# Kernel optimization log

Measured on AMD Instinct MI355X. Metric: run time of the kernel, lower is better.

Reference implementation:

```python
import jax, jax.numpy as jnp
import numpy as np

WS = 8
NH = 8
EPS = 1e-5

def layer_norm(x, g, b):
    m = jnp.mean(x, axis=-1, keepdims=True)
    v = jnp.mean(jnp.square(x - m), axis=-1, keepdims=True)
    return (x - m) * jax.lax.rsqrt(v + EPS) * g + b

def setup_inputs() -> dict:
    key = jax.random.key(0)
    ks = jax.random.split(key, 12)
    C = 512
    s = 1.0 / np.sqrt(C)
    return {
        "x": jax.random.normal(ks[0], (16, C, 96, 96), dtype=jnp.float32),
        "Wqkv": jax.random.normal(ks[1], (C, 3 * C), dtype=jnp.float32) * s,
        "bqkv": jnp.zeros((3 * C,), dtype=jnp.float32),
        "Wo": jax.random.normal(ks[2], (C, C), dtype=jnp.float32) * s,
        "bo": jnp.zeros((C,), dtype=jnp.float32),
        "g1": jnp.ones((C,), dtype=jnp.float32),
        "beta1": jnp.zeros((C,), dtype=jnp.float32),
        "W1": jax.random.normal(ks[3], (C, C), dtype=jnp.float32) * s,
        "bf1": jnp.zeros((C,), dtype=jnp.float32),
        "W2": jax.random.normal(ks[4], (C, C), dtype=jnp.float32) * s,
        "bf2": jnp.zeros((C,), dtype=jnp.float32),
        "g2": jnp.ones((C,), dtype=jnp.float32),
        "beta2": jnp.zeros((C,), dtype=jnp.float32),
    }

def _block(t, Wqkv, bqkv, Wo, bo, g1, beta1, W1, bf1, W2, bf2, g2, beta2):
    # t: [N, L, C]  (windows of L = ws*ws tokens)
    N, L, C = t.shape
    dh = C // NH
    qkv = t @ Wqkv + bqkv                       # [N, L, 3C]
    q, k, v = jnp.split(qkv, 3, axis=-1)
    q = q.reshape(N, L, NH, dh).transpose(0, 2, 1, 3)  # [N,H,L,dh]
    k = k.reshape(N, L, NH, dh).transpose(0, 2, 1, 3)
    v = v.reshape(N, L, NH, dh).transpose(0, 2, 1, 3)
    scores = jnp.einsum('nhqd,nhkd->nhqk', q, k) / jnp.sqrt(jnp.float32(dh))
    attn = jax.nn.softmax(scores, axis=-1)
    o = jnp.einsum('nhqk,nhkd->nhqd', attn, v)  # [N,H,L,dh]
    o = o.transpose(0, 2, 1, 3).reshape(N, L, C) @ Wo + bo
    x1 = layer_norm(t + o, g1, beta1)
    f = jax.nn.relu(x1 @ W1 + bf1) @ W2 + bf2
    return layer_norm(x1 + f, g2, beta2)

def reference(x, Wqkv, bqkv, Wo, bo, g1, beta1, W1, bf1, W2, bf2, g2, beta2):
    B, C, H, W = x.shape
    ws = WS
    # H, W divisible by ws (pad amounts are 0 for chosen shapes)
    nh, nw = H // ws, W // ws
    xw = x.reshape(B, C, nh, ws, nw, ws)
    xw = xw.transpose(0, 2, 4, 3, 5, 1).reshape(B * nh * nw, ws * ws, C)
    y = _block(xw, Wqkv, bqkv, Wo, bo, g1, beta1, W1, bf1, W2, bf2, g2, beta2)
    y = y.reshape(B, nh, nw, ws, ws, C)
    y = y.transpose(0, 5, 1, 3, 2, 4).reshape(B, C, H, W)
    return y
```

## Files before the change

### kernel.cpp

```cpp
#include <hip/hip_runtime.h>

typedef short short8 __attribute__((ext_vector_type(8)));
typedef float f32x4 __attribute__((ext_vector_type(4)));

#define NWIN 2304
#define CP 520
#define LP2 136
#define VTP 72
#define SMEM_BYTES 124416

static __device__ __forceinline__ unsigned short f2bf(float f) {
  unsigned int u = __float_as_uint(f);
  u += 0x7FFFu + ((u >> 16) & 1u);
  return (unsigned short)(u >> 16);
}
static __device__ __forceinline__ float bf2f(unsigned short s) {
  return __uint_as_float(((unsigned int)s) << 16);
}
static __device__ __forceinline__ f32x4 mfma16(short8 a, short8 b, f32x4 c) {
  return __builtin_amdgcn_mfma_f32_16x16x32_bf16(a, b, c, 0, 0, 0);
}
static __device__ __forceinline__ short8 lds8(const unsigned short* p) {
  return *reinterpret_cast<const short8*>(p);
}

__global__ void transpose_cvt_kernel(const float* __restrict__ in,
                                     unsigned short* __restrict__ out,
                                     int K, int N) {
  __shared__ float tile[32][33];
  int bn = blockIdx.x * 32, bk = blockIdx.y * 32;
  int tx = threadIdx.x & 31, ty = threadIdx.x >> 5;
#pragma unroll
  for (int r = 0; r < 32; r += 8)
    tile[ty + r][tx] = in[(size_t)(bk + ty + r) * N + bn + tx];
  __syncthreads();
#pragma unroll
  for (int r = 0; r < 32; r += 8)
    out[(size_t)(bn + ty + r) * K + bk + tx] = f2bf(tile[tx][ty + r]);
}

__global__ __launch_bounds__(512, 2)
void swin_fused(const float* __restrict__ x,
                const unsigned short* __restrict__ WqkvT,
                const float* __restrict__ bqkv,
                const unsigned short* __restrict__ WoT,
                const float* __restrict__ bo,
                const float* __restrict__ g1, const float* __restrict__ beta1,
                const unsigned short* __restrict__ W1T,
                const float* __restrict__ bf1,
                const unsigned short* __restrict__ W2T,
                const float* __restrict__ bf2,
                const float* __restrict__ g2, const float* __restrict__ beta2,
                float* __restrict__ out) {
  extern __shared__ unsigned char smem[];
  unsigned short* sT  = (unsigned short*)smem;
  unsigned short* sQ  = (unsigned short*)(smem + 66560);
  unsigned short* sK  = (unsigned short*)(smem + 83968);
  unsigned short* sVt = (unsigned short*)(smem + 101376);
  unsigned short* sH  = sK;
  float* sSum  = (float*)(smem + 119808);
  float* sSq   = (float*)(smem + 121856);
  float* sMean = (float*)(smem + 123904);
  float* sRstd = (float*)(smem + 124160);

  const int tid = threadIdx.x;
  const int wvid = tid >> 6, lane = tid & 63;
  const int l16 = lane & 15, lg = lane >> 4;

  const int wid = (blockIdx.x & 7) * 288 + (blockIdx.x >> 3);
  const int b = wid / 144, rem = wid % 144;
  const int h0 = (rem / 12) * 8, w0 = (rem % 12) * 8;
  const float* xb = x + (size_t)b * 512 * 9216 + (size_t)h0 * 96 + w0;
  float* ob = out + (size_t)b * 512 * 9216 + (size_t)h0 * 96 + w0;

  const int c2 = wvid * 16 + l16;
  const int hh = wvid >> 2;
  const int mt4 = wvid & 3;
  const int ycol0 = wvid * 64;

#pragma unroll
  for (int it = 0; it < 16; ++it) {
    int gid = it * 512 + tid;
    int c = gid >> 4, hr = (gid >> 1) & 7, wq = gid & 1;
    float4 v = *reinterpret_cast<const float4*>(xb + (size_t)c * 9216 + hr * 96 + wq * 4);
    int tok = hr * 8 + wq * 4;
    sT[(tok + 0) * CP + c] = f2bf(v.x);
    sT[(tok + 1) * CP + c] = f2bf(v.y);
    sT[(tok + 2) * CP + c] = f2bf(v.z);
    sT[(tok + 3) * CP + c] = f2bf(v.w);
  }
  __syncthreads();

  f32x4 Yacc[4][4] = {};

  for (int hp = 0; hp < 4; ++hp) {
    {
      const unsigned short* bq = WqkvT + (size_t)(hp * 128 + c2) * 512;
      const unsigned short* bk = bq + (size_t)512 * 512;
      const unsigned short* bv = bq + (size_t)1024 * 512;
      f32x4 acc[3][4] = {};
      short8 qw[4], kw[4], vw[4];
#pragma unroll
      for (int p = 0; p < 4; ++p) {
        int ko = p * 32 + lg * 8;
        qw[p] = *(const short8*)(bq + ko);
        kw[p] = *(const short8*)(bk + ko);
        vw[p] = *(const short8*)(bv + ko);
      }
#pragma unroll
      for (int ks = 0; ks < 16; ++ks) {
        const int ko = ks * 32 + lg * 8;
        short8 cq = qw[ks & 3], ck = kw[ks & 3], cv = vw[ks & 3];
        if (ks < 12) {
          int ko2 = (ks + 4) * 32 + lg * 8;
          qw[ks & 3] = *(const short8*)(bq + ko2);
          kw[ks & 3] = *(const short8*)(bk + ko2);
          vw[ks & 3] = *(const short8*)(bv + ko2);
        }
        short8 a0 = lds8(&sT[(l16) * CP + ko]);
        short8 a1 = lds8(&sT[(16 + l16) * CP + ko]);
        short8 a2 = lds8(&sT[(32 + l16) * CP + ko]);
        short8 a3 = lds8(&sT[(48 + l16) * CP + ko]);
        acc[0][0] = mfma16(a0, cq, acc[0][0]);
        acc[0][1] = mfma16(a1, cq, acc[0][1]);
        acc[0][2] = mfma16(a2, cq, acc[0][2]);
        acc[0][3] = mfma16(a3, cq, acc[0][3]);
        acc[1][0] = mfma16(a0, ck, acc[1][0]);
        acc[1][1] = mfma16(a1, ck, acc[1][1]);
        acc[1][2] = mfma16(a2, ck, acc[1][2]);
        acc[1][3] = mfma16(a3, ck, acc[1][3]);
        acc[2][0] = mfma16(a0, cv, acc[2][0]);
        acc[2][1] = mfma16(a1, cv, acc[2][1]);
        acc[2][2] = mfma16(a2, cv, acc[2][2]);
        acc[2][3] = mfma16(a3, cv, acc[2][3]);
      }
      const float bqv = bqkv[hp * 128 + c2];
      const float bkv = bqkv[512 + hp * 128 + c2];
      const float bvv = bqkv[1024 + hp * 128 + c2];
#pragma unroll
      for (int mt = 0; mt < 4; ++mt) {
        int tok0 = mt * 16 + lg * 4;
#pragma unroll
        for (int r = 0; r < 4; ++r) {
          sQ[(tok0 + r) * LP2 + c2] = f2bf((acc[0][mt][r] + bqv) * 0.125f);
          sK[(tok0 + r) * LP2 + c2] = f2bf(acc[1][mt][r] + bkv);
        }
        ushort4 pk;
        pk.x = f2bf(acc[2][mt][0] + bvv);
        pk.y = f2bf(acc[2][mt][1] + bvv);
        pk.z = f2bf(acc[2][mt][2] + bvv);
        pk.w = f2bf(acc[2][mt][3] + bvv);
        *reinterpret_cast<ushort4*>(&sVt[c2 * VTP + tok0]) = pk;
      }
    }
    __syncthreads();

    {
      f32x4 sc[4] = {};
#pragma unroll
      for (int ks = 0; ks < 2; ++ks) {
        int ko = hh * 64 + ks * 32 + lg * 8;
        short8 a  = lds8(&sQ[(mt4 * 16 + l16) * LP2 + ko]);
        short8 b0 = lds8(&sK[(l16) * LP2 + ko]);
        short8 b1 = lds8(&sK[(16 + l16) * LP2 + ko]);
        short8 b2 = lds8(&sK[(32 + l16) * LP2 + ko]);
        short8 b3 = lds8(&sK[(48 + l16) * LP2 + ko]);
        sc[0] = mfma16(a, b0, sc[0]);
        sc[1] = mfma16(a, b1, sc[1]);
        sc[2] = mfma16(a, b2, sc[2]);
        sc[3] = mfma16(a, b3, sc[3]);
      }
#pragma unroll
      for (int r = 0; r < 4; ++r) {
        float m = fmaxf(fmaxf(sc[0][r], sc[1][r]), fmaxf(sc[2][r], sc[3][r]));
        m = fmaxf(m, __shfl_xor(m, 1));
        m = fmaxf(m, __shfl_xor(m, 2));
        m = fmaxf(m, __shfl_xor(m, 4));
        m = fmaxf(m, __shfl_xor(m, 8));
        float e0 = __expf(sc[0][r] - m), e1 = __expf(sc[1][r] - m);
        float e2 = __expf(sc[2][r] - m), e3 = __expf(sc[3][r] - m);
        float s = e0 + e1 + e2 + e3;
        s += __shfl_xor(s, 1);
        s += __shfl_xor(s, 2);
        s += __shfl_xor(s, 4);
        s += __shfl_xor(s, 8);
        float inv = 1.0f / s;
        int row = mt4 * 16 + lg * 4 + r;
        sQ[row * LP2 + hh * 64 + l16]      = f2bf(e0 * inv);
        sQ[row * LP2 + hh * 64 + 16 + l16] = f2bf(e1 * inv);
        sQ[row * LP2 + hh * 64 + 32 + l16] = f2bf(e2 * inv);
        sQ[row * LP2 + hh * 64 + 48 + l16] = f2bf(e3 * inv);
      }
    }

    {
      f32x4 ov[4] = {};
#pragma unroll
      for (int ks = 0; ks < 2; ++ks) {
        int ko = ks * 32 + lg * 8;
        short8 a  = lds8(&sQ[(mt4 * 16 + l16) * LP2 + hh * 64 + ko]);
        short8 b0 = lds8(&sVt[(hh * 64 + l16) * VTP + ko]);
        short8 b1 = lds8(&sVt[(hh * 64 + 16 + l16) * VTP + ko]);
        short8 b2 = lds8(&sVt[(hh * 64 + 32 + l16) * VTP + ko]);
        short8 b3 = lds8(&sVt[(hh * 64 + 48 + l16) * VTP + ko]);
        ov[0] = mfma16(a, b0, ov[0]);
        ov[1] = mfma16(a, b1, ov[1]);
        ov[2] = mfma16(a, b2, ov[2]);
        ov[3] = mfma16(a, b3, ov[3]);
      }
#pragma unroll
      for (int r = 0; r < 4; ++r) {
        int row = mt4 * 16 + lg * 4 + r;
        sQ[row * LP2 + hh * 64 + l16]      = f2bf(ov[0][r]);
        sQ[row * LP2 + hh * 64 + 16 + l16] = f2bf(ov[1][r]);
        sQ[row * LP2 + hh * 64 + 32 + l16] = f2bf(ov[2][r]);
        sQ[row * LP2 + hh * 64 + 48 + l16] = f2bf(ov[3][r]);
      }
    }
    __syncthreads();

    {
      const unsigned short* wo0 = WoT + (size_t)(ycol0 + l16) * 512 + hp * 128;
      short8 wb[4][4];
#pragma unroll
      for (int ks = 0; ks < 4; ++ks)
#pragma unroll
        for (int nt = 0; nt < 4; ++nt)
          wb[ks][nt] = *(const short8*)(wo0 + (size_t)nt * 16 * 512 + ks * 32 + lg * 8);
#pragma unroll
      for (int ks = 0; ks < 4; ++ks) {
        int ko = ks * 32 + lg * 8;
        short8 a0 = lds8(&sQ[(l16) * LP2 + ko]);
        short8 a1 = lds8(&sQ[(16 + l16) * LP2 + ko]);
        short8 a2 = lds8(&sQ[(32 + l16) * LP2 + ko]);
        short8 a3 = lds8(&sQ[(48 + l16) * LP2 + ko]);
#pragma unroll
        for (int nt = 0; nt < 4; ++nt) {
          Yacc[0][nt] = mfma16(a0, wb[ks][nt], Yacc[0][nt]);
          Yacc[1][nt] = mfma16(a1, wb[ks][nt], Yacc[1][nt]);
          Yacc[2][nt] = mfma16(a2, wb[ks][nt], Yacc[2][nt]);
          Yacc[3][nt] = mfma16(a3, wb[ks][nt], Yacc[3][nt]);
        }
      }
    }
    __syncthreads();
  }

  {
#pragma unroll
    for (int nt = 0; nt < 4; ++nt) {
      int col = ycol0 + nt * 16 + l16;
      float bv = bo[col];
#pragma unroll
      for (int mt = 0; mt < 4; ++mt) {
        int row0 = mt * 16 + lg * 4;
#pragma unroll
        for (int r = 0; r < 4; ++r)
          Yacc[mt][nt][r] += bv + bf2f(sT[(row0 + r) * CP + col]);
      }
    }
#pragma unroll
    for (int mt = 0; mt < 4; ++mt) {
#pragma unroll
      for (int r = 0; r < 4; ++r) {
        float s = Yacc[mt][0][r] + Yacc[mt][1][r] + Yacc[mt][2][r] + Yacc[mt][3][r];
        float q = Yacc[mt][0][r] * Yacc[mt][0][r] + Yacc[mt][1][r] * Yacc[mt][1][r] +
                  Yacc[mt][2][r] * Yacc[mt][2][r] + Yacc[mt][3][r] * Yacc[mt][3][r];
        s += __shfl_xor(s, 1); s += __shfl_xor(s, 2);
        s += __shfl_xor(s, 4); s += __shfl_xor(s, 8);
        q += __shfl_xor(q, 1); q += __shfl_xor(q, 2);
        q += __shfl_xor(q, 4); q += __shfl_xor(q, 8);
        if (l16 == 0) {
          sSum[wvid * 64 + mt * 16 + lg * 4 + r] = s;
          sSq[wvid * 64 + mt * 16 + lg * 4 + r] = q;
        }
      }
    }
    __syncthreads();
    if (tid < 64) {
      float s = 0.f, q = 0.f;
#pragma unroll
      for (int w = 0; w < 8; ++w) { s += sSum[w * 64 + tid]; q += sSq[w * 64 + tid]; }
      float mean = s * (1.0f / 512.0f);
      float var = q * (1.0f / 512.0f) - mean * mean;
      sMean[tid] = mean;
      sRstd[tid] = rsqrtf(var + 1e-5f);
    }
    __syncthreads();
#pragma unroll
    for (int nt = 0; nt < 4; ++nt) {
      int col = ycol0 + nt * 16 + l16;
      float gv = g1[col], bv = beta1[col];
#pragma unroll
      for (int mt = 0; mt < 4; ++mt) {
        int row0 = mt * 16 + lg * 4;
#pragma unroll
        for (int r = 0; r < 4; ++r) {
          float xv = (Yacc[mt][nt][r] - sMean[row0 + r]) * sRstd[row0 + r] * gv + bv;
          sT[(row0 + r) * CP + col] = f2bf(xv);
        }
      }
    }
  }
  __syncthreads();

  f32x4 Facc[4][4] = {};
  for (int hc = 0; hc < 4; ++hc) {
    {
      const int hcol = hc * 128 + c2;
      const unsigned short* w1p = W1T + (size_t)hcol * 512;
      f32x4 u[4] = {};
      short8 wbuf[4];
#pragma unroll
      for (int p = 0; p < 4; ++p)
        wbuf[p] = *(const short8*)(w1p + p * 32 + lg * 8);
#pragma unroll
      for (int ks = 0; ks < 16; ++ks) {
        int ko = ks * 32 + lg * 8;
        short8 cw = wbuf[ks & 3];
        if (ks < 12)
          wbuf[ks & 3] = *(const short8*)(w1p + (ks + 4) * 32 + lg * 8);
        short8 a0 = lds8(&sT[(l16) * CP + ko]);
        short8 a1 = lds8(&sT[(16 + l16) * CP + ko]);
        short8 a2 = lds8(&sT[(32 + l16) * CP + ko]);
        short8 a3 = lds8(&sT[(48 + l16) * CP + ko]);
        u[0] = mfma16(a0, cw, u[0]);
        u[1] = mfma16(a1, cw, u[1]);
        u[2] = mfma16(a2, cw, u[2]);
        u[3] = mfma16(a3, cw, u[3]);
      }
      float bv = bf1[hcol];
#pragma unroll
      for (int mt = 0; mt < 4; ++mt) {
        int tok0 = mt * 16 + lg * 4;
#pragma unroll
        for (int r = 0; r < 4; ++r)
          sH[(tok0 + r) * LP2 + c2] = f2bf(fmaxf(u[mt][r] + bv, 0.0f));
      }
    }
    __syncthreads();
    {
      const unsigned short* w2p = W2T + (size_t)(ycol0 + l16) * 512 + hc * 128;
      short8 wb[4][4];
#pragma unroll
      for (int ks = 0; ks < 4; ++ks)
#pragma unroll
        for (int nt = 0; nt < 4; ++nt)
          wb[ks][nt] = *(const short8*)(w2p + (size_t)nt * 16 * 512 + ks * 32 + lg * 8);
#pragma unroll
      for (int ks = 0; ks < 4; ++ks) {
        int ko = ks * 32 + lg * 8;
        short8 a0 = lds8(&sH[(l16) * LP2 + ko]);
        short8 a1 = lds8(&sH[(16 + l16) * LP2 + ko]);
        short8 a2 = lds8(&sH[(32 + l16) * LP2 + ko]);
        short8 a3 = lds8(&sH[(48 + l16) * LP2 + ko]);
#pragma unroll
        for (int nt = 0; nt < 4; ++nt) {
          Facc[0][nt] = mfma16(a0, wb[ks][nt], Facc[0][nt]);
          Facc[1][nt] = mfma16(a1, wb[ks][nt], Facc[1][nt]);
          Facc[2][nt] = mfma16(a2, wb[ks][nt], Facc[2][nt]);
          Facc[3][nt] = mfma16(a3, wb[ks][nt], Facc[3][nt]);
        }
      }
    }
    __syncthreads();
  }

  {
#pragma unroll
    for (int nt = 0; nt < 4; ++nt) {
      int col = ycol0 + nt * 16 + l16;
      float bv = bf2[col];
#pragma unroll
      for (int mt = 0; mt < 4; ++mt) {
        int row0 = mt * 16 + lg * 4;
#pragma unroll
        for (int r = 0; r < 4; ++r)
          Facc[mt][nt][r] += bv + bf2f(sT[(row0 + r) * CP + col]);
      }
    }
#pragma unroll
    for (int mt = 0; mt < 4; ++mt) {
#pragma unroll
      for (int r = 0; r < 4; ++r) {
        float s = Facc[mt][0][r] + Facc[mt][1][r] + Facc[mt][2][r] + Facc[mt][3][r];
        float q = Facc[mt][0][r] * Facc[mt][0][r] + Facc[mt][1][r] * Facc[mt][1][r] +
                  Facc[mt][2][r] * Facc[mt][2][r] + Facc[mt][3][r] * Facc[mt][3][r];
        s += __shfl_xor(s, 1); s += __shfl_xor(s, 2);
        s += __shfl_xor(s, 4); s += __shfl_xor(s, 8);
        q += __shfl_xor(q, 1); q += __shfl_xor(q, 2);
        q += __shfl_xor(q, 4); q += __shfl_xor(q, 8);
        if (l16 == 0) {
          sSum[wvid * 64 + mt * 16 + lg * 4 + r] = s;
          sSq[wvid * 64 + mt * 16 + lg * 4 + r] = q;
        }
      }
    }
    __syncthreads();
    if (tid < 64) {
      float s = 0.f, q = 0.f;
#pragma unroll
      for (int w = 0; w < 8; ++w) { s += sSum[w * 64 + tid]; q += sSq[w * 64 + tid]; }
      float mean = s * (1.0f / 512.0f);
      float var = q * (1.0f / 512.0f) - mean * mean;
      sMean[tid] = mean;
      sRstd[tid] = rsqrtf(var + 1e-5f);
    }
    __syncthreads();
#pragma unroll
    for (int nt = 0; nt < 4; ++nt) {
      int col = ycol0 + nt * 16 + l16;
      float gv = g2[col], bv = beta2[col];
      float* op = ob + (size_t)col * 9216;
#pragma unroll
      for (int mt = 0; mt < 4; ++mt) {
        int tok0 = mt * 16 + lg * 4;
        float4 o4;
        o4.x = (Facc[mt][nt][0] - sMean[tok0 + 0]) * sRstd[tok0 + 0] * gv + bv;
        o4.y = (Facc[mt][nt][1] - sMean[tok0 + 1]) * sRstd[tok0 + 1] * gv + bv;
        o4.z = (Facc[mt][nt][2] - sMean[tok0 + 2]) * sRstd[tok0 + 2] * gv + bv;
        o4.w = (Facc[mt][nt][3] - sMean[tok0 + 3]) * sRstd[tok0 + 3] * gv + bv;
        *reinterpret_cast<float4*>(&op[(tok0 >> 3) * 96 + (tok0 & 7)]) = o4;
      }
    }
  }
}

extern "C" void kernel_launch(void* const* d_in, const int* in_sizes, int n_in,
                              void* d_out, int out_size, void* d_ws, size_t ws_size,
                              hipStream_t stream) {
  const float* x     = (const float*)d_in[0];
  const float* Wqkv  = (const float*)d_in[1];
  const float* bqkv  = (const float*)d_in[2];
  const float* Wo    = (const float*)d_in[3];
  const float* bo    = (const float*)d_in[4];
  const float* g1    = (const float*)d_in[5];
  const float* beta1 = (const float*)d_in[6];
  const float* W1    = (const float*)d_in[7];
  const float* bf1   = (const float*)d_in[8];
  const float* W2    = (const float*)d_in[9];
  const float* bf2   = (const float*)d_in[10];
  const float* g2    = (const float*)d_in[11];
  const float* beta2 = (const float*)d_in[12];
  float* out = (float*)d_out;

  unsigned short* ws = (unsigned short*)d_ws;
  unsigned short* WqkvT = ws;
  unsigned short* WoT   = ws + (size_t)1536 * 512;
  unsigned short* W1T   = WoT + (size_t)512 * 512;
  unsigned short* W2T   = W1T + (size_t)512 * 512;

  transpose_cvt_kernel<<<dim3(48, 16), 256, 0, stream>>>(Wqkv, WqkvT, 512, 1536);
  transpose_cvt_kernel<<<dim3(16, 16), 256, 0, stream>>>(Wo, WoT, 512, 512);
  transpose_cvt_kernel<<<dim3(16, 16), 256, 0, stream>>>(W1, W1T, 512, 512);
  transpose_cvt_kernel<<<dim3(16, 16), 256, 0, stream>>>(W2, W2T, 512, 512);

  (void)hipFuncSetAttribute((const void*)swin_fused,
                            hipFuncAttributeMaxDynamicSharedMemorySize, SMEM_BYTES);
  swin_fused<<<NWIN, 512, SMEM_BYTES, stream>>>(x, WqkvT, bqkv, WoT, bo, g1, beta1,
                                                W1T, bf1, W2T, bf2, g2, beta2, out);
}
```

Before: 1.174 ms.

## Shrink LDS footprint with XOR swizzles and half-width streamed input tiles

```diff
diff --git a/kernel.cpp b/kernel.cpp
--- a/kernel.cpp
+++ b/kernel.cpp
@@ -4,10 +4,7 @@
 typedef float f32x4 __attribute__((ext_vector_type(4)));
 
 #define NWIN 2304
-#define CP 520
-#define LP2 136
-#define VTP 72
-#define SMEM_BYTES 124416
+#define SMEM_BYTES 81920
 
 static __device__ __forceinline__ unsigned short f2bf(float f) {
   unsigned int u = __float_as_uint(f);
@@ -22,6 +19,18 @@
 }
 static __device__ __forceinline__ short8 lds8(const unsigned short* p) {
   return *reinterpret_cast<const short8*>(p);
+}
+static __device__ __forceinline__ int swzH(int r, int c) {
+  return r * 256 + ((((c >> 3) ^ (r & 7)) << 3) | (c & 7));
+}
+static __device__ __forceinline__ int swzT(int r, int c) {
+  return r * 512 + ((((c >> 3) ^ (r & 7)) << 3) | (c & 7));
+}
+static __device__ __forceinline__ int swz128(int r, int c) {
+  return r * 128 + ((((c >> 3) ^ (r & 7)) << 3) | (c & 7));
+}
+static __device__ __forceinline__ int swzV(int r, int c) {
+  return r * 64 + ((((c >> 3) ^ (r & 7)) << 3) | (c & 7));
 }
 
 __global__ void transpose_cvt_kernel(const float* __restrict__ in,
@@ -53,15 +62,16 @@
                 const float* __restrict__ g2, const float* __restrict__ beta2,
                 float* __restrict__ out) {
   extern __shared__ unsigned char smem[];
-  unsigned short* sT  = (unsigned short*)smem;
-  unsigned short* sQ  = (unsigned short*)(smem + 66560);
-  unsigned short* sK  = (unsigned short*)(smem + 83968);
-  unsigned short* sVt = (unsigned short*)(smem + 101376);
-  unsigned short* sH  = sK;
-  float* sSum  = (float*)(smem + 119808);
-  float* sSq   = (float*)(smem + 121856);
-  float* sMean = (float*)(smem + 123904);
-  float* sRstd = (float*)(smem + 124160);
+  unsigned short* sTh = (unsigned short*)smem;
+  unsigned short* sQ  = (unsigned short*)(smem + 32768);
+  unsigned short* sK  = (unsigned short*)(smem + 49152);
+  unsigned short* sVt = (unsigned short*)(smem + 65536);
+  unsigned short* sX1 = (unsigned short*)smem;
+  unsigned short* sU  = sVt;
+  float* sSum  = (float*)(smem + 65536);
+  float* sSq   = (float*)(smem + 67584);
+  float* sMean = (float*)(smem + 69632);
+  float* sRstd = (float*)(smem + 69888);
 
   const int tid = threadIdx.x;
   const int wvid = tid >> 6, lane = tid & 63;
@@ -78,49 +88,50 @@
   const int mt4 = wvid & 3;
   const int ycol0 = wvid * 64;
 
-#pragma unroll
-  for (int it = 0; it < 16; ++it) {
-    int gid = it * 512 + tid;
-    int c = gid >> 4, hr = (gid >> 1) & 7, wq = gid & 1;
-    float4 v = *reinterpret_cast<const float4*>(xb + (size_t)c * 9216 + hr * 96 + wq * 4);
-    int tok = hr * 8 + wq * 4;
-    sT[(tok + 0) * CP + c] = f2bf(v.x);
-    sT[(tok + 1) * CP + c] = f2bf(v.y);
-    sT[(tok + 2) * CP + c] = f2bf(v.z);
-    sT[(tok + 3) * CP + c] = f2bf(v.w);
-  }
-  __syncthreads();
-
   f32x4 Yacc[4][4] = {};
 
   for (int hp = 0; hp < 4; ++hp) {
-    {
-      const unsigned short* bq = WqkvT + (size_t)(hp * 128 + c2) * 512;
+    f32x4 acc[3][4] = {};
+    const unsigned short* bq0 = WqkvT + (size_t)(hp * 128 + c2) * 512;
+    for (int kh = 0; kh < 2; ++kh) {
+#pragma unroll
+      for (int it = 0; it < 8; ++it) {
+        int gid = it * 512 + tid;
+        int c = gid >> 4, hr = (gid >> 1) & 7, wq = gid & 1;
+        float4 v = *reinterpret_cast<const float4*>(
+            xb + (size_t)(kh * 256 + c) * 9216 + hr * 96 + wq * 4);
+        int tok = hr * 8 + wq * 4;
+        sTh[swzH(tok + 0, c)] = f2bf(v.x);
+        sTh[swzH(tok + 1, c)] = f2bf(v.y);
+        sTh[swzH(tok + 2, c)] = f2bf(v.z);
+        sTh[swzH(tok + 3, c)] = f2bf(v.w);
+      }
+      __syncthreads();
+      const unsigned short* bq = bq0 + kh * 256;
       const unsigned short* bk = bq + (size_t)512 * 512;
       const unsigned short* bv = bq + (size_t)1024 * 512;
-      f32x4 acc[3][4] = {};
-      short8 qw[4], kw[4], vw[4];
-#pragma unroll
-      for (int p = 0; p < 4; ++p) {
+      short8 qw[2], kw[2], vw[2];
+#pragma unroll
+      for (int p = 0; p < 2; ++p) {
         int ko = p * 32 + lg * 8;
         qw[p] = *(const short8*)(bq + ko);
         kw[p] = *(const short8*)(bk + ko);
         vw[p] = *(const short8*)(bv + ko);
       }
 #pragma unroll
-      for (int ks = 0; ks < 16; ++ks) {
+      for (int ks = 0; ks < 8; ++ks) {
         const int ko = ks * 32 + lg * 8;
-        short8 cq = qw[ks & 3], ck = kw[ks & 3], cv = vw[ks & 3];
-        if (ks < 12) {
-          int ko2 = (ks + 4) * 32 + lg * 8;
-          qw[ks & 3] = *(const short8*)(bq + ko2);
-          kw[ks & 3] = *(const short8*)(bk + ko2);
-          vw[ks & 3] = *(const short8*)(bv + ko2);
-        }
-        short8 a0 = lds8(&sT[(l16) * CP + ko]);
-        short8 a1 = lds8(&sT[(16 + l16) * CP + ko]);
-        short8 a2 = lds8(&sT[(32 + l16) * CP + ko]);
-        short8 a3 = lds8(&sT[(48 + l16) * CP + ko]);
+        short8 cq = qw[ks & 1], ck = kw[ks & 1], cv = vw[ks & 1];
+        if (ks < 6) {
+          int k2 = (ks + 2) * 32 + lg * 8;
+          qw[ks & 1] = *(const short8*)(bq + k2);
+          kw[ks & 1] = *(const short8*)(bk + k2);
+          vw[ks & 1] = *(const short8*)(bv + k2);
+        }
+        short8 a0 = lds8(sTh + swzH(l16, ko));
+        short8 a1 = lds8(sTh + swzH(16 + l16, ko));
+        short8 a2 = lds8(sTh + swzH(32 + l16, ko));
+        short8 a3 = lds8(sTh + swzH(48 + l16, ko));
         acc[0][0] = mfma16(a0, cq, acc[0][0]);
         acc[0][1] = mfma16(a1, cq, acc[0][1]);
         acc[0][2] = mfma16(a2, cq, acc[0][2]);
@@ -134,6 +145,9 @@
         acc[2][2] = mfma16(a2, cv, acc[2][2]);
         acc[2][3] = mfma16(a3, cv, acc[2][3]);
       }
+      __syncthreads();
+    }
+    {
       const float bqv = bqkv[hp * 128 + c2];
       const float bkv = bqkv[512 + hp * 128 + c2];
       const float bvv = bqkv[1024 + hp * 128 + c2];
@@ -142,15 +156,15 @@
         int tok0 = mt * 16 + lg * 4;
 #pragma unroll
         for (int r = 0; r < 4; ++r) {
-          sQ[(tok0 + r) * LP2 + c2] = f2bf((acc[0][mt][r] + bqv) * 0.125f);
-          sK[(tok0 + r) * LP2 + c2] = f2bf(acc[1][mt][r] + bkv);
+          sQ[swz128(tok0 + r, c2)] = f2bf((acc[0][mt][r] + bqv) * 0.125f);
+          sK[swz128(tok0 + r, c2)] = f2bf(acc[1][mt][r] + bkv);
         }
         ushort4 pk;
         pk.x = f2bf(acc[2][mt][0] + bvv);
         pk.y = f2bf(acc[2][mt][1] + bvv);
         pk.z = f2bf(acc[2][mt][2] + bvv);
         pk.w = f2bf(acc[2][mt][3] + bvv);
-        *reinterpret_cast<ushort4*>(&sVt[c2 * VTP + tok0]) = pk;
+        *reinterpret_cast<ushort4*>(sVt + swzV(c2, tok0)) = pk;
       }
     }
     __syncthreads();
@@ -159,12 +173,12 @@
       f32x4 sc[4] = {};
 #pragma unroll
       for (int ks = 0; ks < 2; ++ks) {
-        int ko = hh * 64 + ks * 32 + lg * 8;
-        short8 a  = lds8(&sQ[(mt4 * 16 + l16) * LP2 + ko]);
-        short8 b0 = lds8(&sK[(l16) * LP2 + ko]);
-        short8 b1 = lds8(&sK[(16 + l16) * LP2 + ko]);
-        short8 b2 = lds8(&sK[(32 + l16) * LP2 + ko]);
-        short8 b3 = lds8(&sK[(48 + l16) * LP2 + ko]);
+        int kb = hh * 64 + ks * 32 + lg * 8;
+        short8 a  = lds8(sQ + swz128(mt4 * 16 + l16, kb));
+        short8 b0 = lds8(sK + swz128(l16, kb));
+        short8 b1 = lds8(sK + swz128(16 + l16, kb));
+        short8 b2 = lds8(sK + swz128(32 + l16, kb));
+        short8 b3 = lds8(sK + swz128(48 + l16, kb));
         sc[0] = mfma16(a, b0, sc[0]);
         sc[1] = mfma16(a, b1, sc[1]);
         sc[2] = mfma16(a, b2, sc[2]);
@@ -186,10 +200,10 @@
         s += __shfl_xor(s, 8);
         float inv = 1.0f / s;
         int row = mt4 * 16 + lg * 4 + r;
-        sQ[row * LP2 + hh * 64 + l16]      = f2bf(e0 * inv);
-        sQ[row * LP2 + hh * 64 + 16 + l16] = f2bf(e1 * inv);
-        sQ[row * LP2 + hh * 64 + 32 + l16] = f2bf(e2 * inv);
-        sQ[row * LP2 + hh * 64 + 48 + l16] = f2bf(e3 * inv);
+        sQ[swz128(row, hh * 64 + l16)]      = f2bf(e0 * inv);
+        sQ[swz128(row, hh * 64 + 16 + l16)] = f2bf(e1 * inv);
+        sQ[swz128(row, hh * 64 + 32 + l16)] = f2bf(e2 * inv);
+        sQ[swz128(row, hh * 64 + 48 + l16)] = f2bf(e3 * inv);
       }
     }
 
@@ -197,12 +211,12 @@
       f32x4 ov[4] = {};
 #pragma unroll
       for (int ks = 0; ks < 2; ++ks) {
-        int ko = ks * 32 + lg * 8;
-        short8 a  = lds8(&sQ[(mt4 * 16 + l16) * LP2 + hh * 64 + ko]);
-        short8 b0 = lds8(&sVt[(hh * 64 + l16) * VTP + ko]);
-        short8 b1 = lds8(&sVt[(hh * 64 + 16 + l16) * VTP + ko]);
-        short8 b2 = lds8(&sVt[(hh * 64 + 32 + l16) * VTP + ko]);
-        short8 b3 = lds8(&sVt[(hh * 64 + 48 + l16) * VTP + ko]);
+        int kb = ks * 32 + lg * 8;
+        short8 a  = lds8(sQ + swz128(mt4 * 16 + l16, hh * 64 + kb));
+        short8 b0 = lds8(sVt + swzV(hh * 64 + l16, kb));
+        short8 b1 = lds8(sVt + swzV(hh * 64 + 16 + l16, kb));
+        short8 b2 = lds8(sVt + swzV(hh * 64 + 32 + l16, kb));
+        short8 b3 = lds8(sVt + swzV(hh * 64 + 48 + l16, kb));
         ov[0] = mfma16(a, b0, ov[0]);
         ov[1] = mfma16(a, b1, ov[1]);
         ov[2] = mfma16(a, b2, ov[2]);
@@ -211,35 +225,40 @@
 #pragma unroll
       for (int r = 0; r < 4; ++r) {
         int row = mt4 * 16 + lg * 4 + r;
-        sQ[row * LP2 + hh * 64 + l16]      = f2bf(ov[0][r]);
-        sQ[row * LP2 + hh * 64 + 16 + l16] = f2bf(ov[1][r]);
-        sQ[row * LP2 + hh * 64 + 32 + l16] = f2bf(ov[2][r]);
-        sQ[row * LP2 + hh * 64 + 48 + l16] = f2bf(ov[3][r]);
-      }
-    }
-    __syncthreads();
-
-    {
-      const unsigned short* wo0 = WoT + (size_t)(ycol0 + l16) * 512 + hp * 128;
-      short8 wb[4][4];
-#pragma unroll
-      for (int ks = 0; ks < 4; ++ks)
+        sQ[swz128(row, hh * 64 + l16)]      = f2bf(ov[0][r]);
+        sQ[swz128(row, hh * 64 + 16 + l16)] = f2bf(ov[1][r]);
+        sQ[swz128(row, hh * 64 + 32 + l16)] = f2bf(ov[2][r]);
+        sQ[swz128(row, hh * 64 + 48 + l16)] = f2bf(ov[3][r]);
+      }
+    }
+    __syncthreads();
+
+    {
+      const unsigned short* wo[4];
+#pragma unroll
+      for (int nt = 0; nt < 4; ++nt)
+        wo[nt] = WoT + (size_t)(ycol0 + nt * 16 + l16) * 512 + hp * 128;
+      short8 wb[2][4];
+#pragma unroll
+      for (int p = 0; p < 2; ++p)
 #pragma unroll
         for (int nt = 0; nt < 4; ++nt)
-          wb[ks][nt] = *(const short8*)(wo0 + (size_t)nt * 16 * 512 + ks * 32 + lg * 8);
+          wb[p][nt] = *(const short8*)(wo[nt] + p * 32 + lg * 8);
 #pragma unroll
       for (int ks = 0; ks < 4; ++ks) {
         int ko = ks * 32 + lg * 8;
-        short8 a0 = lds8(&sQ[(l16) * LP2 + ko]);
-        short8 a1 = lds8(&sQ[(16 + l16) * LP2 + ko]);
-        short8 a2 = lds8(&sQ[(32 + l16) * LP2 + ko]);
-        short8 a3 = lds8(&sQ[(48 + l16) * LP2 + ko]);
+        short8 a0 = lds8(sQ + swz128(l16, ko));
+        short8 a1 = lds8(sQ + swz128(16 + l16, ko));
+        short8 a2 = lds8(sQ + swz128(32 + l16, ko));
+        short8 a3 = lds8(sQ + swz128(48 + l16, ko));
 #pragma unroll
         for (int nt = 0; nt < 4; ++nt) {
-          Yacc[0][nt] = mfma16(a0, wb[ks][nt], Yacc[0][nt]);
-          Yacc[1][nt] = mfma16(a1, wb[ks][nt], Yacc[1][nt]);
-          Yacc[2][nt] = mfma16(a2, wb[ks][nt], Yacc[2][nt]);
-          Yacc[3][nt] = mfma16(a3, wb[ks][nt], Yacc[3][nt]);
+          short8 w = wb[ks & 1][nt];
+          if (ks < 2) wb[ks & 1][nt] = *(const short8*)(wo[nt] + (ks + 2) * 32 + lg * 8);
+          Yacc[0][nt] = mfma16(a0, w, Yacc[0][nt]);
+          Yacc[1][nt] = mfma16(a1, w, Yacc[1][nt]);
+          Yacc[2][nt] = mfma16(a2, w, Yacc[2][nt]);
+          Yacc[3][nt] = mfma16(a3, w, Yacc[3][nt]);
         }
       }
     }
@@ -251,12 +270,15 @@
     for (int nt = 0; nt < 4; ++nt) {
       int col = ycol0 + nt * 16 + l16;
       float bv = bo[col];
+      const float* xc = xb + (size_t)col * 9216;
 #pragma unroll
       for (int mt = 0; mt < 4; ++mt) {
         int row0 = mt * 16 + lg * 4;
-#pragma unroll
-        for (int r = 0; r < 4; ++r)
-          Yacc[mt][nt][r] += bv + bf2f(sT[(row0 + r) * CP + col]);
+        float4 xv = *reinterpret_cast<const float4*>(xc + (row0 >> 3) * 96 + (row0 & 7));
+        Yacc[mt][nt][0] += bv + xv.x;
+        Yacc[mt][nt][1] += bv + xv.y;
+        Yacc[mt][nt][2] += bv + xv.z;
+        Yacc[mt][nt][3] += bv + xv.w;
       }
     }
 #pragma unroll
@@ -297,7 +319,7 @@
 #pragma unroll
         for (int r = 0; r < 4; ++r) {
           float xv = (Yacc[mt][nt][r] - sMean[row0 + r]) * sRstd[row0 + r] * gv + bv;
-          sT[(row0 + r) * CP + col] = f2bf(xv);
+          sX1[swzT(row0 + r, col)] = f2bf(xv);
         }
       }
     }
@@ -310,20 +332,19 @@
       const int hcol = hc * 128 + c2;
       const unsigned short* w1p = W1T + (size_t)hcol * 512;
       f32x4 u[4] = {};
-      short8 wbuf[4];
-#pragma unroll
-      for (int p = 0; p < 4; ++p)
-        wbuf[p] = *(const short8*)(w1p + p * 32 + lg * 8);
+      short8 wbuf[2];
+      wbuf[0] = *(const short8*)(w1p + lg * 8);
+      wbuf[1] = *(const short8*)(w1p + 32 + lg * 8);
 #pragma unroll
       for (int ks = 0; ks < 16; ++ks) {
         int ko = ks * 32 + lg * 8;
-        short8 cw = wbuf[ks & 3];
-        if (ks < 12)
-          wbuf[ks & 3] = *(const short8*)(w1p + (ks + 4) * 32 + lg * 8);
-        short8 a0 = lds8(&sT[(l16) * CP + ko]);
-        short8 a1 = lds8(&sT[(16 + l16) * CP + ko]);
-        short8 a2 = lds8(&sT[(32 + l16) * CP + ko]);
-        short8 a3 = lds8(&sT[(48 + l16) * CP + ko]);
+        short8 cw = wbuf[ks & 1];
+        if (ks < 14)
+          wbuf[ks & 1] = *(const short8*)(w1p + (ks + 2) * 32 + lg * 8);
+        short8 a0 = lds8(sX1 + swzT(l16, ko));
+        short8 a1 = lds8(sX1 + swzT(16 + l16, ko));
+        short8 a2 = lds8(sX1 + swzT(32 + l16, ko));
+        short8 a3 = lds8(sX1 + swzT(48 + l16, ko));
         u[0] = mfma16(a0, cw, u[0]);
         u[1] = mfma16(a1, cw, u[1]);
         u[2] = mfma16(a2, cw, u[2]);
@@ -335,31 +356,36 @@
         int tok0 = mt * 16 + lg * 4;
 #pragma unroll
         for (int r = 0; r < 4; ++r)
-          sH[(tok0 + r) * LP2 + c2] = f2bf(fmaxf(u[mt][r] + bv, 0.0f));
-      }
-    }
-    __syncthreads();
-    {
-      const unsigned short* w2p = W2T + (size_t)(ycol0 + l16) * 512 + hc * 128;
-      short8 wb[4][4];
-#pragma unroll
-      for (int ks = 0; ks < 4; ++ks)
+          sU[swz128(tok0 + r, c2)] = f2bf(fmaxf(u[mt][r] + bv, 0.0f));
+      }
+    }
+    __syncthreads();
+    {
+      const unsigned short* w2[4];
+#pragma unroll
+      for (int nt = 0; nt < 4; ++nt)
+        w2[nt] = W2T + (size_t)(ycol0 + nt * 16 + l16) * 512 + hc * 128;
+      short8 wb[2][4];
+#pragma unroll
+      for (int p = 0; p < 2; ++p)
 #pragma unroll
         for (int nt = 0; nt < 4; ++nt)
-          wb[ks][nt] = *(const short8*)(w2p + (size_t)nt * 16 * 512 + ks * 32 + lg * 8);
+          wb[p][nt] = *(const short8*)(w2[nt] + p * 32 + lg * 8);
 #pragma unroll
       for (int ks = 0; ks < 4; ++ks) {
         int ko = ks * 32 + lg * 8;
-        short8 a0 = lds8(&sH[(l16) * LP2 + ko]);
-        short8 a1 = lds8(&sH[(16 + l16) * LP2 + ko]);
-        short8 a2 = lds8(&sH[(32 + l16) * LP2 + ko]);
-        short8 a3 = lds8(&sH[(48 + l16) * LP2 + ko]);
+        short8 a0 = lds8(sU + swz128(l16, ko));
+        short8 a1 = lds8(sU + swz128(16 + l16, ko));
+        short8 a2 = lds8(sU + swz128(32 + l16, ko));
+        short8 a3 = lds8(sU + swz128(48 + l16, ko));
 #pragma unroll
         for (int nt = 0; nt < 4; ++nt) {
-          Facc[0][nt] = mfma16(a0, wb[ks][nt], Facc[0][nt]);
-          Facc[1][nt] = mfma16(a1, wb[ks][nt], Facc[1][nt]);
-          Facc[2][nt] = mfma16(a2, wb[ks][nt], Facc[2][nt]);
-          Facc[3][nt] = mfma16(a3, wb[ks][nt], Facc[3][nt]);
+          short8 w = wb[ks & 1][nt];
+          if (ks < 2) wb[ks & 1][nt] = *(const short8*)(w2[nt] + (ks + 2) * 32 + lg * 8);
+          Facc[0][nt] = mfma16(a0, w, Facc[0][nt]);
+          Facc[1][nt] = mfma16(a1, w, Facc[1][nt]);
+          Facc[2][nt] = mfma16(a2, w, Facc[2][nt]);
+          Facc[3][nt] = mfma16(a3, w, Facc[3][nt]);
         }
       }
     }
@@ -376,7 +402,7 @@
         int row0 = mt * 16 + lg * 4;
 #pragma unroll
         for (int r = 0; r < 4; ++r)
-          Facc[mt][nt][r] += bv + bf2f(sT[(row0 + r) * CP + col]);
+          Facc[mt][nt][r] += bv + bf2f(sX1[swzT(row0 + r, col)]);
       }
     }
 #pragma unroll
@@ -414,13 +440,13 @@
       float* op = ob + (size_t)col * 9216;
 #pragma unroll
       for (int mt = 0; mt < 4; ++mt) {
-        int tok0 = mt * 16 + lg * 4;
+        int t0 = mt * 16 + lg * 4;
         float4 o4;
-        o4.x = (Facc[mt][nt][0] - sMean[tok0 + 0]) * sRstd[tok0 + 0] * gv + bv;
-        o4.y = (Facc[mt][nt][1] - sMean[tok0 + 1]) * sRstd[tok0 + 1] * gv + bv;
-        o4.z = (Facc[mt][nt][2] - sMean[tok0 + 2]) * sRstd[tok0 + 2] * gv + bv;
-        o4.w = (Facc[mt][nt][3] - sMean[tok0 + 3]) * sRstd[tok0 + 3] * gv + bv;
-        *reinterpret_cast<float4*>(&op[(tok0 >> 3) * 96 + (tok0 & 7)]) = o4;
+        o4.x = (Facc[mt][nt][0] - sMean[t0 + 0]) * sRstd[t0 + 0] * gv + bv;
+        o4.y = (Facc[mt][nt][1] - sMean[t0 + 1]) * sRstd[t0 + 1] * gv + bv;
+        o4.z = (Facc[mt][nt][2] - sMean[t0 + 2]) * sRstd[t0 + 2] * gv + bv;
+        o4.w = (Facc[mt][nt][3] - sMean[t0 + 3]) * sRstd[t0 + 3] * gv + bv;
+        *reinterpret_cast<float4*>(op + (t0 >> 3) * 96 + (t0 & 7)) = o4;
       }
     }
   }
```

After: 1.588 ms. +35.2%, slower.
